# Kernel tuning notes

Hardware: AMD Instinct MI355X
Metric: run time of the kernel (lower is better)

The kernel has to match this reference:

```python
import jax, jax.numpy as jnp
import numpy as np

N_WIRES = 4
DIM = 16          # 2**N_WIRES
QDEPTH = 2
IN_C = 4
OUT_C = 16
K0 = K1 = 3
PAD = 1
# PennyLane StronglyEntanglingLayers default ranges for n_wires>1
RANGES = [(l % (N_WIRES - 1)) + 1 for l in range(QDEPTH)]


def _mottonen_ry(state, a):
    """Apply Mottonen state-prep RY cascade (real non-negative amplitudes a).
    state: (N, 16) complex64; a: (N, 16) float, l2-normalized, >= 0."""
    n = N_WIRES
    a2 = a * a
    for k in range(n, 0, -1):
        t = n - k  # target wire (0 = MSB), controls are wires 0..t-1
        blocks = a2.reshape(-1, 2 ** t, 2, 2 ** (k - 1))
        num = blocks[:, :, 1, :].sum(-1)
        den = blocks.sum(axis=(-2, -1))
        safe = den > 1e-20
        ratio = jnp.sqrt(jnp.where(safe, num / jnp.where(safe, den, 1.0), 0.0))
        alpha = 2.0 * jnp.arcsin(jnp.clip(ratio, 0.0, 1.0))  # (N, 2^t)
        c = jnp.cos(alpha * 0.5)[..., None].astype(state.dtype)
        s = jnp.sin(alpha * 0.5)[..., None].astype(state.dtype)
        st = state.reshape(-1, 2 ** t, 2, 2 ** (n - t - 1))
        s0, s1 = st[:, :, 0, :], st[:, :, 1, :]
        state = jnp.stack([c * s0 - s * s1, s * s0 + c * s1], axis=2).reshape(state.shape)
    return state


def _rot_matrix(phi, theta, omega):
    # qml.Rot = RZ(omega) @ RY(theta) @ RZ(phi)
    ct, st = jnp.cos(theta * 0.5), jnp.sin(theta * 0.5)
    ep = jnp.exp(-0.5j * (phi + omega))
    em = jnp.exp(0.5j * (phi - omega))
    row0 = jnp.stack([ep * ct, -em * st])
    row1 = jnp.stack([jnp.conj(em) * st, jnp.conj(ep) * ct])
    return jnp.stack([row0, row1]).astype(jnp.complex64)


def _apply_1q(state, mat, w):
    st = state.reshape(-1, 2 ** w, 2, 2 ** (N_WIRES - w - 1))
    st = jnp.einsum('ab,npbq->npaq', mat, st)
    return st.reshape(state.shape)


def _apply_cnot(state, c, t):
    st = state.reshape((-1,) + (2,) * N_WIRES)
    st = jnp.moveaxis(st, (1 + c, 1 + t), (1, 2))
    st = jnp.stack([st[:, 0], st[:, 1, ::-1]], axis=1)
    st = jnp.moveaxis(st, (1, 2), (1 + c, 1 + t))
    return st.reshape(state.shape)


def _forward(x, weights):
    b, c, h, w = x.shape
    h_out = h + 2 * PAD - K0 + 1
    w_out = w + 2 * PAD - K1 + 1
    xp = jnp.pad(x, ((0, 0), (0, 0), (PAD, PAD), (PAD, PAD)), constant_values=0.01)
    # (b, c, h_out, w_out, k0*k1) patches, k0-major like torch unfold
    patches = jnp.stack([xp[:, :, i:i + h_out, j:j + w_out]
                         for i in range(K0) for j in range(K1)], axis=-1)
    patches = patches.transpose(0, 2, 3, 1, 4).reshape(b * h_out * w_out, c, K0 * K1)
    patches = jnp.pad(patches, ((0, 0), (0, 0), (0, DIM - K0 * K1)))
    norm = jnp.linalg.norm(patches, axis=-1, keepdims=True)
    a = patches / jnp.maximum(norm, 1e-12)  # (N, c, 16), non-negative
    N = a.shape[0]
    state = jnp.zeros((N, DIM), dtype=jnp.complex64).at[:, 0].set(1.0)
    for ic in range(c):
        state = _mottonen_ry(state, a[:, ic])
        for l in range(QDEPTH):
            for wq in range(N_WIRES):
                phi, theta, omega = weights[ic, l, wq]
                state = _apply_1q(state, _rot_matrix(phi, theta, omega), wq)
            r = RANGES[l]
            for i in range(N_WIRES):
                state = _apply_cnot(state, i, (i + r) % N_WIRES)
    probs = state.real ** 2 + state.imag ** 2  # (N, 16)
    out = jnp.clip(probs * (DIM * 0.5), 0.0, 1.0)[:, :OUT_C]
    return out.reshape(b, h_out, w_out, OUT_C).transpose(0, 3, 1, 2)


def setup_inputs() -> dict:
    key = jax.random.key(0)
    k1, k2 = jax.random.split(key)
    x = jax.random.uniform(k1, (32, IN_C, 64, 64), dtype=jnp.float32)
    weights = jax.random.uniform(k2, (IN_C, QDEPTH, N_WIRES, 3), dtype=jnp.float32)
    return {"x": x, "weights": weights}


def reference(x, weights):
    return _forward(x, weights)
```

## Files before the change

### kernel.cpp

```cpp
#include <hip/hip_runtime.h>


typedef float     f2      __attribute__((ext_vector_type(2)));
typedef __fp16    fp16x2  __attribute__((ext_vector_type(2)));
typedef _Float16  half8_t __attribute__((ext_vector_type(8)));
typedef float     f32x16  __attribute__((ext_vector_type(16)));

union H8 { fp16x2 h2[4]; half8_t h8; };

__device__ __forceinline__ f2 pkfma(f2 a, f2 b, f2 c) {
    return __builtin_elementwise_fma(a, b, c);
}
__device__ __forceinline__ f2 swap2(f2 v) {
    return __builtin_shufflevector(v, v, 1, 0);
}

struct GateM { f2 m00rr, m00ni, m01rr, m01ni, m10rr, m10ni, m11rr, m11ni; };

__device__ __forceinline__ GateM load_gate(const float* gp) {
    const float4* p = (const float4*)gp;
    const float4 e0 = p[0], e1 = p[1], e2 = p[2], e3 = p[3];
    GateM G;
    G.m00rr = f2{e0.x, e0.y}; G.m00ni = f2{e0.z, e0.w};
    G.m01rr = f2{e1.x, e1.y}; G.m01ni = f2{e1.z, e1.w};
    G.m10rr = f2{e2.x, e2.y}; G.m10ni = f2{e2.z, e2.w};
    G.m11rr = f2{e3.x, e3.y}; G.m11ni = f2{e3.z, e3.w};
    return G;
}

template<int STRIDE>
__device__ __forceinline__ void apply_gate(f2* s, const GateM G) {
    #pragma unroll
    for (int m0 = 0; m0 < 16; ++m0) {
        if (m0 & STRIDE) continue;
        const int m1 = m0 | STRIDE;
        const f2 a = s[m0], b = s[m1];
        const f2 as = swap2(a), bs = swap2(b);
        f2 o0 = G.m00rr * a;
        o0 = pkfma(G.m00ni, as, o0);
        o0 = pkfma(G.m01rr, b,  o0);
        o0 = pkfma(G.m01ni, bs, o0);
        f2 o1 = G.m10rr * a;
        o1 = pkfma(G.m10ni, as, o1);
        o1 = pkfma(G.m11rr, b,  o1);
        o1 = pkfma(G.m11ni, bs, o1);
        s[m0] = o0; s[m1] = o1;
    }
}

template<int BC, int BT>
__device__ __forceinline__ void apply_cnot(f2* s) {
    #pragma unroll
    for (int m = 0; m < 16; ++m) {
        if ((m & BC) && !(m & BT)) {
            const int m2 = m | BT;
            const f2 t = s[m]; s[m] = s[m2]; s[m2] = t;
        }
    }
}

__device__ __forceinline__ void node_cs(float lo, float hi_, float& c, float& s) {
    const float den = lo + hi_;
    const bool ok = den > 1e-30f;
    const float rs = __builtin_amdgcn_rsqf(fmaxf(den, 1e-37f));
    c = ok ? __builtin_amdgcn_sqrtf(lo)  * rs : 1.0f;
    s = ok ? __builtin_amdgcn_sqrtf(hi_) * rs : 0.0f;
}

#define ROTP(a, b, c, s) { \
    const float _na = fmaf((c), (a), -((s) * (b))); \
    const float _nb = fmaf((s), (a),  ((c) * (b))); \
    (a) = _na; (b) = _nb; }

__global__ __launch_bounds__(256, 4) void qconv_kernel(
        const float* __restrict__ x,
        const float* __restrict__ wts,
        float* __restrict__ out) {
    __shared__ float   smat[32 * 16];
    __shared__ float   tile[4 * 4 * 64];
    __shared__ f2      ucol[4 * 16 * 16];
    __shared__ half8_t ufrag[4 * 2 * 64];

    const int tid = threadIdx.x;
    const int blk = blockIdx.x;
    const int b  = blk >> 5;
    const int ry = blk & 31;

    const float* xb = x + (size_t)b * 16384;
    #pragma unroll
    for (int i = 0; i < 4; ++i) {
        const int e = tid + i * 256;
        const int r = e >> 8, ch = (e >> 6) & 3, col = e & 63;
        const int gy = 2 * ry - 1 + r;
        const int gyc = min(max(gy, 0), 63);
        float val = xb[ch * 4096 + gyc * 64 + col];
        val = ((unsigned)gy < 64u) ? val : 0.01f;
        tile[e] = val;
    }

    if (tid < 32) {
        const float phi   = wts[tid*3 + 0];
        const float theta = wts[tid*3 + 1];
        const float omega = wts[tid*3 + 2];
        float st, ct; __sincosf(0.5f * theta,         &st, &ct);
        float sA, cA; __sincosf(0.5f * (phi + omega), &sA, &cA);
        float sB, cB; __sincosf(0.5f * (phi - omega), &sB, &cB);
        float* g = &smat[tid * 16];
        g[0]  =  cA*ct; g[1]  =  cA*ct; g[2]  =  sA*ct; g[3]  = -sA*ct;
        g[4]  = -cB*st; g[5]  = -cB*st; g[6]  =  sB*st; g[7]  = -sB*st;
        g[8]  =  cB*st; g[9]  =  cB*st; g[10] =  sB*st; g[11] = -sB*st;
        g[12] =  cA*ct; g[13] =  cA*ct; g[14] = -sA*ct; g[15] =  sA*ct;
    }
    __syncthreads();

    if (tid < 64) {
        const int ch = tid >> 4, col = tid & 15;
        f2 u[16];
        #pragma unroll
        for (int j = 0; j < 16; ++j)
            u[j] = (j == col) ? f2{1.f, 0.f} : f2{0.f, 0.f};
        const float* cb = smat + ch * 128;
        apply_gate<8>(u, load_gate(cb + 0*16));
        apply_gate<4>(u, load_gate(cb + 1*16));
        apply_gate<2>(u, load_gate(cb + 2*16));
        apply_gate<1>(u, load_gate(cb + 3*16));
        apply_cnot<8, 4>(u); apply_cnot<4, 2>(u);
        apply_cnot<2, 1>(u); apply_cnot<1, 8>(u);
        apply_gate<8>(u, load_gate(cb + 4*16));
        apply_gate<4>(u, load_gate(cb + 5*16));
        apply_gate<2>(u, load_gate(cb + 6*16));
        apply_gate<1>(u, load_gate(cb + 7*16));
        apply_cnot<8, 2>(u); apply_cnot<4, 1>(u);
        apply_cnot<2, 8>(u); apply_cnot<1, 4>(u);
        #pragma unroll
        for (int j = 0; j < 16; ++j)
            ucol[(ch * 16 + col) * 16 + j] = u[j];
    }
    __syncthreads();

    {
        const int ch = tid >> 6, l = tid & 63;
        const int m = l & 31, hif = l >> 5;
        const bool mi = m >= 16;
        const int mr = m & 15;
        #pragma unroll
        for (int ks = 0; ks < 2; ++ks) {
            half8_t f;
            #pragma unroll
            for (int i = 0; i < 8; ++i) {
                const int amp = 4 * hif + (i & 3) + 8 * (i >> 2);
                const f2 e = ucol[(ch * 16 + amp) * 16 + mr];
                const float val = mi ? (ks ? e.x : e.y) : (ks ? -e.y : e.x);
                f[i] = (_Float16)val;
            }
            ufrag[(ch * 2 + ks) * 64 + l] = f;
        }
    }
    __syncthreads();

    const int w = tid >> 6, lane = tid & 63;
    const int hi = lane >> 5;
    const int row = 2 * ry + (w >> 1);
    const int xc = ((w & 1) << 5) + (lane & 31);
    const int colm = min(max(xc - 1, 0), 63);
    const int colp = min(xc + 1, 63);
    const bool inm = xc > 0, inp = xc < 63;
    const int tr0 = (w >> 1);

    float v[16];
    #pragma unroll
    for (int i = 0; i < 16; ++i) v[i] = 0.f;
    v[0] = hi ? 0.f : 1.f;

    #pragma unroll
    for (int ic = 0; ic < 4; ++ic) {
        const half8_t A0 = ufrag[(ic * 2 + 0) * 64 + lane];
        const half8_t A1 = ufrag[(ic * 2 + 1) * 64 + lane];

        float q[9];
        #pragma unroll
        for (int dy = 0; dy < 3; ++dy) {
            const float* rowp = tile + ((tr0 + dy) * 4 + ic) * 64;
            float vm = rowp[colm]; vm = inm ? vm : 0.01f;
            float v0 = rowp[xc];
            float vp = rowp[colp]; vp = inp ? vp : 0.01f;
            q[dy*3 + 0] = vm * vm;
            q[dy*3 + 1] = v0 * v0;
            q[dy*3 + 2] = vp * vp;
        }

        const float s01 = q[0]+q[1], s23 = q[2]+q[3];
        const float s45 = q[4]+q[5], s67 = q[6]+q[7];
        const float s03 = s01+s23, s47 = s45+s67, s07 = s03+s47;
        const float i2lo = hi ? s45  : s01,  i2hi = hi ? s67  : s23;
        const float i3xl = hi ? q[4] : q[0], i3xh = hi ? q[5] : q[1];
        const float i3yl = hi ? q[6] : q[2], i3yh = hi ? q[7] : q[3];
        float c0,s0,c1,s1,c2e,s2e,c3x,s3x,c3y,s3y;
        node_cs(s07,  q[8], c0,  s0);
        node_cs(s03,  s47,  c1,  s1);
        node_cs(i2lo, i2hi, c2e, s2e);
        node_cs(i3xl, i3xh, c3x, s3x);
        node_cs(i3yl, i3yh, c3y, s3y);
        const float bs1 = hi ? s1 : -s1;

        #pragma unroll
        for (int k = 0; k < 4; ++k) {
            ROTP(v[k],   v[k+4],  c0, s0);
            ROTP(v[k+8], v[k+12], c0, s0);
        }
        float rr[4], ri[4];
        #pragma unroll
        for (int k = 0; k < 4; ++k) rr[k] = __shfl_xor(v[k],   32);
        #pragma unroll
        for (int k = 0; k < 4; ++k) ri[k] = __shfl_xor(v[8+k], 32);
        #pragma unroll
        for (int k = 0; k < 4; ++k) {
            v[k]   = fmaf(c1, v[k],   bs1 * rr[k]);
            v[8+k] = fmaf(c1, v[8+k], bs1 * ri[k]);
        }
        ROTP(v[0], v[2],  c2e, s2e);  ROTP(v[1], v[3],  c2e, s2e);
        ROTP(v[8], v[10], c2e, s2e);  ROTP(v[9], v[11], c2e, s2e);
        ROTP(v[0], v[1],  c3x, s3x);  ROTP(v[2], v[3],   c3y, s3y);
        ROTP(v[8], v[9],  c3x, s3x);  ROTP(v[10], v[11], c3y, s3y);

        H8 b0, b1;
        b0.h2[0] = __builtin_amdgcn_cvt_pkrtz(v[0],  v[1]);
        b0.h2[1] = __builtin_amdgcn_cvt_pkrtz(v[2],  v[3]);
        b0.h2[2] = __builtin_amdgcn_cvt_pkrtz(v[4],  v[5]);
        b0.h2[3] = __builtin_amdgcn_cvt_pkrtz(v[6],  v[7]);
        b1.h2[0] = __builtin_amdgcn_cvt_pkrtz(v[8],  v[9]);
        b1.h2[1] = __builtin_amdgcn_cvt_pkrtz(v[10], v[11]);
        b1.h2[2] = __builtin_amdgcn_cvt_pkrtz(v[12], v[13]);
        b1.h2[3] = __builtin_amdgcn_cvt_pkrtz(v[14], v[15]);

        f32x16 acc;
        #pragma unroll
        for (int i = 0; i < 16; ++i) acc[i] = 0.f;
        acc = __builtin_amdgcn_mfma_f32_32x32x16_f16(A0, b0.h8, acc, 0, 0, 0);
        acc = __builtin_amdgcn_mfma_f32_32x32x16_f16(A1, b1.h8, acc, 0, 0, 0);
        #pragma unroll
        for (int i = 0; i < 16; ++i) v[i] = acc[i];
    }

    float* ob = out + (size_t)b * 65536 + (size_t)row * 64 + xc;
    #pragma unroll
    for (int k = 0; k < 4; ++k) {
        const float plo = v[k]   * v[k]   + v[8+k]  * v[8+k];
        const float phi = v[4+k] * v[4+k] + v[12+k] * v[12+k];
        ob[(4*hi + k) * 4096]     = fminf(plo * 8.f, 1.f);
        ob[(8 + 4*hi + k) * 4096] = fminf(phi * 8.f, 1.f);
    }
}

extern "C" void kernel_launch(void* const* d_in, const int* in_sizes, int n_in,
                              void* d_out, int out_size, void* d_ws, size_t ws_size,
                              hipStream_t stream) {
    const float* x   = (const float*)d_in[0];
    const float* wts = (const float*)d_in[1];
    float* out = (float*)d_out;
    qconv_kernel<<<1024, 256, 0, stream>>>(x, wts, out);
}
```

Baseline: 16.45 us.

## Interleave real/imag in MFMA layout to use packed FMA rotations

Reorders the unitary fragment rows so the MFMA accumulator holds each amplitude's real and imaginary parts in adjacent registers. The Mottonen RY rotations can then run as packed f2 FMAs instead of scalar FMAs. It also simplifies node_cs by dropping the branch and select guard in favour of a tiny epsilon. The aim is fewer VALU instructions per channel, at the cost of a slightly different degenerate-case behaviour when a denominator is zero.

```diff
diff --git a/kernel.cpp b/kernel.cpp
--- a/kernel.cpp
+++ b/kernel.cpp
@@ -6,7 +6,8 @@
 typedef _Float16  half8_t __attribute__((ext_vector_type(8)));
 typedef float     f32x16  __attribute__((ext_vector_type(16)));
 
-union H8 { fp16x2 h2[4]; half8_t h8; };
+union H8  { fp16x2 h2[4]; half8_t h8; };
+union AccW { f32x16 a; f2 w[8]; };
 
 __device__ __forceinline__ f2 pkfma(f2 a, f2 b, f2 c) {
     return __builtin_elementwise_fma(a, b, c);
@@ -60,16 +61,15 @@
 }
 
 __device__ __forceinline__ void node_cs(float lo, float hi_, float& c, float& s) {
-    const float den = lo + hi_;
-    const bool ok = den > 1e-30f;
-    const float rs = __builtin_amdgcn_rsqf(fmaxf(den, 1e-37f));
-    c = ok ? __builtin_amdgcn_sqrtf(lo)  * rs : 1.0f;
-    s = ok ? __builtin_amdgcn_sqrtf(hi_) * rs : 0.0f;
-}
-
-#define ROTP(a, b, c, s) { \
-    const float _na = fmaf((c), (a), -((s) * (b))); \
-    const float _nb = fmaf((s), (a),  ((c) * (b))); \
+    const float lo2 = lo + 1e-30f;
+    const float r = __builtin_amdgcn_rsqf(lo2 + hi_);
+    c = __builtin_amdgcn_sqrtf(lo2) * r;
+    s = __builtin_amdgcn_sqrtf(hi_) * r;
+}
+
+#define PKROT(a, b, cc, ss) { \
+    const f2 _na = __builtin_elementwise_fma(cc, a, -((ss) * (b))); \
+    const f2 _nb = __builtin_elementwise_fma(ss, a,  ((cc) * (b))); \
     (a) = _na; (b) = _nb; }
 
 __global__ __launch_bounds__(256, 4) void qconv_kernel(
@@ -140,37 +140,41 @@
 
     {
         const int ch = tid >> 6, l = tid & 63;
-        const int m = l & 31, hif = l >> 5;
-        const bool mi = m >= 16;
-        const int mr = m & 15;
-        #pragma unroll
-        for (int ks = 0; ks < 2; ++ks) {
+        const int mrow = l & 31, kf = l >> 5;
+        const int hr = (mrow >> 2) & 1;
+        const int ii = (mrow & 3) | ((mrow >> 3) << 2);
+        const int jj = ii >> 1, pr = ii & 1;
+        const int amp_out = (jj < 4) ? 4*hr + jj : 4*hr + jj + 4;
+        #pragma unroll
+        for (int m = 0; m < 2; ++m) {
             half8_t f;
             #pragma unroll
             for (int i = 0; i < 8; ++i) {
-                const int amp = 4 * hif + (i & 3) + 8 * (i >> 2);
-                const f2 e = ucol[(ch * 16 + amp) * 16 + mr];
-                const float val = mi ? (ks ? e.x : e.y) : (ks ? -e.y : e.x);
+                const int n = i >> 1, pk = i & 1;
+                const int jin = 4*m + n;
+                const int amp_in = (jin < 4) ? 4*kf + jin : 4*kf + jin + 4;
+                const f2 e = ucol[(ch * 16 + amp_in) * 16 + amp_out];
+                const float val = pr ? (pk ? e.x : e.y) : (pk ? -e.y : e.x);
                 f[i] = (_Float16)val;
             }
-            ufrag[(ch * 2 + ks) * 64 + l] = f;
+            ufrag[(ch * 2 + m) * 64 + l] = f;
         }
     }
     __syncthreads();
 
-    const int w = tid >> 6, lane = tid & 63;
+    const int wv = tid >> 6, lane = tid & 63;
     const int hi = lane >> 5;
-    const int row = 2 * ry + (w >> 1);
-    const int xc = ((w & 1) << 5) + (lane & 31);
+    const int row = 2 * ry + (wv >> 1);
+    const int xc = ((wv & 1) << 5) + (lane & 31);
     const int colm = min(max(xc - 1, 0), 63);
     const int colp = min(xc + 1, 63);
     const bool inm = xc > 0, inp = xc < 63;
-    const int tr0 = (w >> 1);
-
-    float v[16];
-    #pragma unroll
-    for (int i = 0; i < 16; ++i) v[i] = 0.f;
-    v[0] = hi ? 0.f : 1.f;
+    const int tr0 = (wv >> 1);
+
+    AccW S;
+    #pragma unroll
+    for (int j = 0; j < 8; ++j) S.w[j] = f2{0.f, 0.f};
+    S.w[0].x = hi ? 0.f : 1.f;
 
     #pragma unroll
     for (int ic = 0; ic < 4; ++ic) {
@@ -203,52 +207,51 @@
         node_cs(i3yl, i3yh, c3y, s3y);
         const float bs1 = hi ? s1 : -s1;
 
-        #pragma unroll
-        for (int k = 0; k < 4; ++k) {
-            ROTP(v[k],   v[k+4],  c0, s0);
-            ROTP(v[k+8], v[k+12], c0, s0);
-        }
-        float rr[4], ri[4];
-        #pragma unroll
-        for (int k = 0; k < 4; ++k) rr[k] = __shfl_xor(v[k],   32);
-        #pragma unroll
-        for (int k = 0; k < 4; ++k) ri[k] = __shfl_xor(v[8+k], 32);
-        #pragma unroll
-        for (int k = 0; k < 4; ++k) {
-            v[k]   = fmaf(c1, v[k],   bs1 * rr[k]);
-            v[8+k] = fmaf(c1, v[8+k], bs1 * ri[k]);
-        }
-        ROTP(v[0], v[2],  c2e, s2e);  ROTP(v[1], v[3],  c2e, s2e);
-        ROTP(v[8], v[10], c2e, s2e);  ROTP(v[9], v[11], c2e, s2e);
-        ROTP(v[0], v[1],  c3x, s3x);  ROTP(v[2], v[3],   c3y, s3y);
-        ROTP(v[8], v[9],  c3x, s3x);  ROTP(v[10], v[11], c3y, s3y);
+        const f2 c0f = f2{c0, c0},   s0f = f2{s0, s0};
+        const f2 c1f = f2{c1, c1},   b1f = f2{bs1, bs1};
+        const f2 c2f = f2{c2e, c2e}, s2f = f2{s2e, s2e};
+        const f2 c3xf = f2{c3x, c3x}, s3xf = f2{s3x, s3x};
+        const f2 c3yf = f2{c3y, c3y}, s3yf = f2{s3y, s3y};
+
+        PKROT(S.w[0], S.w[4], c0f, s0f);
+        PKROT(S.w[1], S.w[5], c0f, s0f);
+        PKROT(S.w[2], S.w[6], c0f, s0f);
+        PKROT(S.w[3], S.w[7], c0f, s0f);
+        f2 p[4];
+        #pragma unroll
+        for (int j = 0; j < 4; ++j) {
+            p[j].x = __shfl_xor(S.w[j].x, 32);
+            p[j].y = __shfl_xor(S.w[j].y, 32);
+        }
+        #pragma unroll
+        for (int j = 0; j < 4; ++j)
+            S.w[j] = __builtin_elementwise_fma(c1f, S.w[j], b1f * p[j]);
+        PKROT(S.w[0], S.w[2], c2f, s2f);
+        PKROT(S.w[1], S.w[3], c2f, s2f);
+        PKROT(S.w[0], S.w[1], c3xf, s3xf);
+        PKROT(S.w[2], S.w[3], c3yf, s3yf);
 
         H8 b0, b1;
-        b0.h2[0] = __builtin_amdgcn_cvt_pkrtz(v[0],  v[1]);
-        b0.h2[1] = __builtin_amdgcn_cvt_pkrtz(v[2],  v[3]);
-        b0.h2[2] = __builtin_amdgcn_cvt_pkrtz(v[4],  v[5]);
-        b0.h2[3] = __builtin_amdgcn_cvt_pkrtz(v[6],  v[7]);
-        b1.h2[0] = __builtin_amdgcn_cvt_pkrtz(v[8],  v[9]);
-        b1.h2[1] = __builtin_amdgcn_cvt_pkrtz(v[10], v[11]);
-        b1.h2[2] = __builtin_amdgcn_cvt_pkrtz(v[12], v[13]);
-        b1.h2[3] = __builtin_amdgcn_cvt_pkrtz(v[14], v[15]);
+        #pragma unroll
+        for (int n = 0; n < 4; ++n) {
+            b0.h2[n] = __builtin_amdgcn_cvt_pkrtz(S.w[n].x,     S.w[n].y);
+            b1.h2[n] = __builtin_amdgcn_cvt_pkrtz(S.w[4 + n].x, S.w[4 + n].y);
+        }
 
         f32x16 acc;
         #pragma unroll
         for (int i = 0; i < 16; ++i) acc[i] = 0.f;
         acc = __builtin_amdgcn_mfma_f32_32x32x16_f16(A0, b0.h8, acc, 0, 0, 0);
         acc = __builtin_amdgcn_mfma_f32_32x32x16_f16(A1, b1.h8, acc, 0, 0, 0);
-        #pragma unroll
-        for (int i = 0; i < 16; ++i) v[i] = acc[i];
+        S.a = acc;
     }
 
     float* ob = out + (size_t)b * 65536 + (size_t)row * 64 + xc;
     #pragma unroll
-    for (int k = 0; k < 4; ++k) {
-        const float plo = v[k]   * v[k]   + v[8+k]  * v[8+k];
-        const float phi = v[4+k] * v[4+k] + v[12+k] * v[12+k];
-        ob[(4*hi + k) * 4096]     = fminf(plo * 8.f, 1.f);
-        ob[(8 + 4*hi + k) * 4096] = fminf(phi * 8.f, 1.f);
+    for (int j = 0; j < 8; ++j) {
+        const int amp = (j < 4) ? 4*hi + j : 4*hi + j + 4;
+        const float pr = S.w[j].x * S.w[j].x + S.w[j].y * S.w[j].y;
+        ob[amp * 4096] = fminf(pr * 8.f, 1.f);
     }
 }
 
```

Result: faster. 14.83 us (-9.8%).
